# Kernel tuning notes

Measured on AMD Instinct MI355X. Metric: run time of the kernel, lower is better.

## Reference

```python
import jax, jax.numpy as jnp
import numpy as np

B, C, W, H = 4, 256, 64, 64
CQ = C // 8


def setup_inputs() -> dict:
    key = jax.random.key(0)
    ks = jax.random.split(key, 8)
    s = 1.0 / np.sqrt(C)
    return {
        "x": jax.random.normal(ks[0], (B, C, W, H), dtype=jnp.float32),
        "Wq": jax.random.normal(ks[1], (CQ, C), dtype=jnp.float32) * s,
        "bq": jnp.zeros((CQ,), dtype=jnp.float32),
        "Wk": jax.random.normal(ks[2], (CQ, C), dtype=jnp.float32) * s,
        "bk": jnp.zeros((CQ,), dtype=jnp.float32),
        "Wv": jax.random.normal(ks[3], (C, C), dtype=jnp.float32) * s,
        "bv": jnp.zeros((C,), dtype=jnp.float32),
        "gamma": jnp.zeros((1,), dtype=jnp.float32),
    }


def reference(x, Wq, bq, Wk, bk, Wv, bv, gamma):
    b, c, w, h = x.shape
    n = w * h
    xf = x.reshape(b, c, n)  # [B, C, N] flattened spatial
    # 1x1 convs are channel-wise linear maps
    q = jnp.einsum("dc,bcn->bnd", Wq, xf) + bq  # [B, N, C//8]
    k = jnp.einsum("dc,bcn->bdn", Wk, xf) + bk[None, :, None]  # [B, C//8, N]
    v = jnp.einsum("dc,bcn->bdn", Wv, xf) + bv[None, :, None]  # [B, C, N]
    attn = jax.nn.softmax(jnp.einsum("bnd,bdm->bnm", q, k), axis=-1)  # [B, N, N]
    # out[b, c, n] = sum_m v[b, c, m] * attn[b, n, m]
    out = jnp.einsum("bdm,bnm->bdn", v, attn).reshape(b, c, w, h)
    return gamma[0] * out + x
```

## Files before the change

kernel.cpp:

```cpp
#include <hip/hip_runtime.h>
#include <hip/hip_bf16.h>

#define CC 256
#define NN 4096
#define CQ 32
#define LOG2E 1.4426950408889634f

using short4v = __attribute__((ext_vector_type(4))) short;
using short8 = __attribute__((ext_vector_type(8))) short;
using f32x4  = __attribute__((ext_vector_type(4))) float;

static __device__ __forceinline__ short f2bf(float f) {
  __hip_bfloat16 h = __float2bfloat16(f);
  return *reinterpret_cast<short*>(&h);
}

__global__ __launch_bounds__(256) void prep_kernel(
    const float* __restrict__ Wq, const float* __restrict__ Wk,
    const float* __restrict__ Wv, __hip_bfloat16* __restrict__ Wf)
{
  int t = blockIdx.x*256 + threadIdx.x;
  int lane = t & 63, frag = t >> 6;
  int tile = frag >> 3, kc = frag & 7;
  int l15 = lane & 15, quad = lane >> 4;
  int R = tile*16 + l15;
  int k0 = kc*32 + quad*8;
  const float* src;
  if (R < 32)       src = Wq + (size_t)R*CC + k0;
  else if (R < 64)  src = Wk + (size_t)(R-32)*CC + k0;
  else              src = Wv + (size_t)(R-64)*CC + k0;
  float4 a = *(const float4*)(src);
  float4 c = *(const float4*)(src + 4);
  short8 o;
  o[0]=f2bf(a.x); o[1]=f2bf(a.y); o[2]=f2bf(a.z); o[3]=f2bf(a.w);
  o[4]=f2bf(c.x); o[5]=f2bf(c.y); o[6]=f2bf(c.z); o[7]=f2bf(c.w);
  *reinterpret_cast<short8*>(reinterpret_cast<short*>(Wf) + (size_t)t*8) = o;
}

__global__ __launch_bounds__(256) void qkv_kernel(
    const float* __restrict__ x, const __hip_bfloat16* __restrict__ Wf,
    const float* __restrict__ bq, const float* __restrict__ bk,
    const float* __restrict__ bv,
    __hip_bfloat16* __restrict__ qb, __hip_bfloat16* __restrict__ kb,
    __hip_bfloat16* __restrict__ vb)
{
  const int b  = blockIdx.y;
  const int n0 = blockIdx.x * 32;
  const int tid = threadIdx.x;
  const int lane = tid & 63;
  const int w = __builtin_amdgcn_readfirstlane(tid >> 6);
  const int l15 = lane & 15, quad = lane >> 4;

  __shared__ __align__(16) short Xl[16*64*8];
  __shared__ __align__(16) short Vr[4][16][32];

  const float* xb = x + (size_t)b*CC*NN;
#pragma unroll
  for (int i = 0; i < 4; i++) {
    int s = tid + 256*i;
    int g = s >> 6, ln = s & 63;
    int nr = g >> 3, kc = g & 7;
    int l15s = ln & 15, quads = ln >> 4;
    int n = n0 + nr*16 + l15s;
    int c0 = kc*32 + quads*8;
    float v[8];
#pragma unroll
    for (int j = 0; j < 8; j++) v[j] = xb[(size_t)(c0 + j)*NN + n];
    short8 sv;
#pragma unroll
    for (int j = 0; j < 8; j++) sv[j] = f2bf(v[j]);
    *reinterpret_cast<short8*>(&Xl[(size_t)s*8]) = sv;
  }
  __syncthreads();

  const short* wfp = reinterpret_cast<const short*>(Wf);
  short* qb_s = reinterpret_cast<short*>(qb) + (size_t)b*NN*CQ;
  short* kb_s = reinterpret_cast<short*>(kb) + (size_t)b*NN*CQ;
  short* vb_s = reinterpret_cast<short*>(vb) + (size_t)b*CC*NN;

#define QKV_TILE(T) { \
    const int t_ = (T); \
    short8 Af[8]; \
    _Pragma("unroll") \
    for (int kc = 0; kc < 8; kc++) \
      Af[kc] = *(const short8*)(wfp + ((size_t)(t_*8 + kc)*64 + lane)*8); \
    f32x4 ac0 = {0.f,0.f,0.f,0.f}, ac1 = {0.f,0.f,0.f,0.f}; \
    _Pragma("unroll") \
    for (int kc = 0; kc < 8; kc++) { \
      short8 B0 = *(const short8*)(&Xl[((     kc)*64 + lane)*8]); \
      short8 B1 = *(const short8*)(&Xl[((8 +  kc)*64 + lane)*8]); \
      ac0 = __builtin_amdgcn_mfma_f32_16x16x32_bf16(Af[kc], B0, ac0, 0,0,0); \
      ac1 = __builtin_amdgcn_mfma_f32_16x16x32_bf16(Af[kc], B1, ac1, 0,0,0); \
    } \
    if (t_ < 2) { \
      int d0 = t_*16 + quad*4; \
      short4v p0, p1; \
      _Pragma("unroll") \
      for (int r = 0; r < 4; r++) { \
        float bb = bq[d0 + r]; \
        p0[r] = f2bf(LOG2E*(ac0[r] + bb)); \
        p1[r] = f2bf(LOG2E*(ac1[r] + bb)); \
      } \
      *(short4v*)(qb_s + (size_t)(n0      + l15)*CQ + d0) = p0; \
      *(short4v*)(qb_s + (size_t)(n0 + 16 + l15)*CQ + d0) = p1; \
    } else if (t_ < 4) { \
      int d0 = (t_-2)*16 + quad*4; \
      short4v p0, p1; \
      _Pragma("unroll") \
      for (int r = 0; r < 4; r++) { \
        float bb = bk[d0 + r]; \
        p0[r] = f2bf(ac0[r] + bb); \
        p1[r] = f2bf(ac1[r] + bb); \
      } \
      *(short4v*)(kb_s + (size_t)(n0      + l15)*CQ + d0) = p0; \
      *(short4v*)(kb_s + (size_t)(n0 + 16 + l15)*CQ + d0) = p1; \
    } else { \
      int rv0 = (t_-4)*16; \
      _Pragma("unroll") \
      for (int r = 0; r < 4; r++) { \
        float bb = bv[rv0 + quad*4 + r]; \
        Vr[w][quad*4 + r][     l15] = f2bf(ac0[r] + bb); \
        Vr[w][quad*4 + r][16 + l15] = f2bf(ac1[r] + bb); \
      } \
      int row = lane >> 2, cb = (lane & 3)*8; \
      short8 tv = *(const short8*)(&Vr[w][row][cb]); \
      *(short8*)(vb_s + (size_t)(rv0 + row)*NN + n0 + cb) = tv; \
    } }

  QKV_TILE(w);
  QKV_TILE(4 + w);
  QKV_TILE(8 + w);
  QKV_TILE(12 + w);
  QKV_TILE(16 + w);
#undef QKV_TILE
}

__global__ __launch_bounds__(512, 2) void attn_kernel(
    const __hip_bfloat16* __restrict__ qb, const __hip_bfloat16* __restrict__ kb,
    const __hip_bfloat16* __restrict__ vb,
    const float* __restrict__ x, const float* __restrict__ gamma,
    float* __restrict__ out)
{
  const int Bk = blockIdx.x;
  const int b = (Bk & 7) >> 1;
  const int n0 = ((Bk >> 3)*2 + (Bk & 1)) * 64;
  const int tid = threadIdx.x;
  const int lane = tid & 63;
  const int w = __builtin_amdgcn_readfirstlane(tid >> 6);
  const int sg = w & 3;
  const int mh = w >> 2;
  const int l15 = lane & 15, quad = lane >> 4;

  __shared__ __align__(16) short Vs[256][72];
  __shared__ __align__(16) short Ps[64][72];
  __shared__ float Lbuf2[2][64];

  const short* qbase = (const short*)qb + (size_t)b*NN*CQ;
  const short* kbase = (const short*)kb + (size_t)b*NN*CQ;
  const short* vbase = (const short*)vb + (size_t)b*CC*NN;

  short8 aq = *(const short8*)(qbase + (size_t)(n0 + sg*16 + l15)*CQ + quad*8);

  const int vr = tid >> 1, sh = tid & 1;

  short8 vf0, vf1, vf2, vf3, kf0, kf1;
#pragma unroll
  for (int j = 0; j < 4; j++) {
    short8 t = *(const short8*)(vbase + (size_t)vr*NN + sh*32 + j*8);
    if (j == 0) vf0 = t; else if (j == 1) vf1 = t; else if (j == 2) vf2 = t; else vf3 = t;
  }
  kf0 = *(const short8*)(kbase + (size_t)(mh*32 +      l15)*CQ + quad*8);
  kf1 = *(const short8*)(kbase + (size_t)(mh*32 + 16 + l15)*CQ + quad*8);
  *(short8*)(&Vs[vr][sh*32 +  0]) = vf0;
  *(short8*)(&Vs[vr][sh*32 +  8]) = vf1;
  *(short8*)(&Vs[vr][sh*32 + 16]) = vf2;
  *(short8*)(&Vs[vr][sh*32 + 24]) = vf3;

  f32x4 acc[4][4];
#pragma unroll
  for (int cg = 0; cg < 4; cg++)
#pragma unroll
    for (int ng = 0; ng < 4; ng++) acc[cg][ng] = (f32x4){0.f,0.f,0.f,0.f};
  float lsum[4] = {0.f,0.f,0.f,0.f};

  __syncthreads();

  for (int T = 0; T < 64; T++) {
    short8 nv0, nv1, nv2, nv3, nk0, nk1;
    if (T < 63) {
      const short* vp = vbase + (size_t)vr*NN + (T+1)*64 + sh*32;
      nv0 = *(const short8*)(vp);
      nv1 = *(const short8*)(vp + 8);
      nv2 = *(const short8*)(vp + 16);
      nv3 = *(const short8*)(vp + 24);
      nk0 = *(const short8*)(kbase + (size_t)((T+1)*64 + mh*32 +      l15)*CQ + quad*8);
      nk1 = *(const short8*)(kbase + (size_t)((T+1)*64 + mh*32 + 16 + l15)*CQ + quad*8);
    }

    f32x4 z = {0.f,0.f,0.f,0.f};
    f32x4 S0 = __builtin_amdgcn_mfma_f32_16x16x32_bf16(aq, kf0, z, 0,0,0);
    f32x4 S1 = __builtin_amdgcn_mfma_f32_16x16x32_bf16(aq, kf1, z, 0,0,0);
#pragma unroll
    for (int r = 0; r < 4; r++) {
      float e0 = __builtin_amdgcn_exp2f(S0[r]);
      float e1 = __builtin_amdgcn_exp2f(S1[r]);
      lsum[r] += e0 + e1;
      Ps[sg*16 + quad*4 + r][mh*32 +      l15] = f2bf(e0);
      Ps[sg*16 + quad*4 + r][mh*32 + 16 + l15] = f2bf(e1);
    }
    __syncthreads();

    short8 ap0 = *(const short8*)(&Ps[     l15][mh*32 + quad*8]);
    short8 ap1 = *(const short8*)(&Ps[16 + l15][mh*32 + quad*8]);
    short8 ap2 = *(const short8*)(&Ps[32 + l15][mh*32 + quad*8]);
    short8 ap3 = *(const short8*)(&Ps[48 + l15][mh*32 + quad*8]);
#pragma unroll
    for (int cg = 0; cg < 4; cg++) {
      short8 av = *(const short8*)(&Vs[sg*64 + cg*16 + l15][mh*32 + quad*8]);
      acc[cg][0] = __builtin_amdgcn_mfma_f32_16x16x32_bf16(av, ap0, acc[cg][0], 0,0,0);
      acc[cg][1] = __builtin_amdgcn_mfma_f32_16x16x32_bf16(av, ap1, acc[cg][1], 0,0,0);
      acc[cg][2] = __builtin_amdgcn_mfma_f32_16x16x32_bf16(av, ap2, acc[cg][2], 0,0,0);
      acc[cg][3] = __builtin_amdgcn_mfma_f32_16x16x32_bf16(av, ap3, acc[cg][3], 0,0,0);
    }
    __syncthreads();

    if (T < 63) {
      *(short8*)(&Vs[vr][sh*32 +  0]) = nv0;
      *(short8*)(&Vs[vr][sh*32 +  8]) = nv1;
      *(short8*)(&Vs[vr][sh*32 + 16]) = nv2;
      *(short8*)(&Vs[vr][sh*32 + 24]) = nv3;
      kf0 = nk0; kf1 = nk1;
    }
  }

#pragma unroll
  for (int r = 0; r < 4; r++) {
    float s = lsum[r];
    s += __shfl_xor(s, 1); s += __shfl_xor(s, 2);
    s += __shfl_xor(s, 4); s += __shfl_xor(s, 8);
    if (l15 == 0) Lbuf2[mh][sg*16 + quad*4 + r] = s;
  }

  float* poolf = reinterpret_cast<float*>(&Vs[0][0]);
  __syncthreads();
#pragma unroll
  for (int g = 0; g < 2; g++) {
    if (mh == 1 && (sg >> 1) == g) {
#pragma unroll
      for (int cg = 0; cg < 4; cg++)
#pragma unroll
        for (int ng = 0; ng < 4; ng++)
#pragma unroll
          for (int r = 0; r < 4; r++)
            poolf[(sg & 1)*4096 + (cg*16 + quad*4 + r)*64 + ng*16 + l15] = acc[cg][ng][r];
    }
    __syncthreads();
    if (mh == 0 && (sg >> 1) == g) {
#pragma unroll
      for (int cg = 0; cg < 4; cg++)
#pragma unroll
        for (int ng = 0; ng < 4; ng++)
#pragma unroll
          for (int r = 0; r < 4; r++)
            acc[cg][ng][r] += poolf[(sg & 1)*4096 + (cg*16 + quad*4 + r)*64 + ng*16 + l15];
    }
    __syncthreads();
  }

  if (mh == 0) {
    const float gm = gamma[0];
    float Lv[4];
#pragma unroll
    for (int ng = 0; ng < 4; ng++)
      Lv[ng] = 1.0f / (Lbuf2[0][ng*16 + l15] + Lbuf2[1][ng*16 + l15]);
#pragma unroll
    for (int cg = 0; cg < 4; cg++) {
#pragma unroll
      for (int ng = 0; ng < 4; ng++) {
#pragma unroll
        for (int r = 0; r < 4; r++) {
          size_t idx = ((size_t)b*CC + sg*64 + cg*16 + quad*4 + r)*NN + n0 + ng*16 + l15;
          out[idx] = gm * acc[cg][ng][r] * Lv[ng] + x[idx];
        }
      }
    }
  }
}

extern "C" void kernel_launch(void* const* d_in, const int* in_sizes, int n_in,
                              void* d_out, int out_size, void* d_ws, size_t ws_size,
                              hipStream_t stream) {
  const float* x     = (const float*)d_in[0];
  const float* Wq    = (const float*)d_in[1];
  const float* bq    = (const float*)d_in[2];
  const float* Wk    = (const float*)d_in[3];
  const float* bk    = (const float*)d_in[4];
  const float* Wv    = (const float*)d_in[5];
  const float* bv    = (const float*)d_in[6];
  const float* gamma = (const float*)d_in[7];
  float* out = (float*)d_out;

  char* ws = (char*)d_ws;
  if (ws_size < (11u << 20)) return;
  __hip_bfloat16* qb = (__hip_bfloat16*)(ws);
  __hip_bfloat16* kb = (__hip_bfloat16*)(ws + (1u << 20));
  __hip_bfloat16* vb = (__hip_bfloat16*)(ws + (2u << 20));
  __hip_bfloat16* Wf = (__hip_bfloat16*)(ws + (10u << 20));

  prep_kernel<<<dim3(40), 256, 0, stream>>>(Wq, Wk, Wv, Wf);
  qkv_kernel<<<dim3(128, 4), 256, 0, stream>>>(x, Wf, bq, bk, bv, qb, kb, vb);
  attn_kernel<<<dim3(256), 512, 0, stream>>>(qb, kb, vb, x, gamma, out);
}
```

Before: 151.6 us.

## Double waves per block in attention and QKV kernels, splitting work further

The attention kernel goes from 8 to 16 waves per block. Each wave now computes scores for 16 key columns instead of 32, and accumulates PV output for half of the 64 query rows. Row sums are reduced from four partial buffers. The QKV projection kernel likewise moves to 512 threads, each wave handling fewer tiles. The intent is better latency hiding and MFMA utilisation, since only about one block lands per CU. The cost is more LDS traffic and barrier participants per tile, plus aggressive launch bounds that may squeeze registers.

```diff
diff --git a/kernel.cpp b/kernel.cpp
--- a/kernel.cpp
+++ b/kernel.cpp
@@ -37,7 +37,7 @@
   *reinterpret_cast<short8*>(reinterpret_cast<short*>(Wf) + (size_t)t*8) = o;
 }
 
-__global__ __launch_bounds__(256) void qkv_kernel(
+__global__ __launch_bounds__(512, 4) void qkv_kernel(
     const float* __restrict__ x, const __hip_bfloat16* __restrict__ Wf,
     const float* __restrict__ bq, const float* __restrict__ bk,
     const float* __restrict__ bv,
@@ -52,12 +52,12 @@
   const int l15 = lane & 15, quad = lane >> 4;
 
   __shared__ __align__(16) short Xl[16*64*8];
-  __shared__ __align__(16) short Vr[4][16][32];
+  __shared__ __align__(16) short Vr[8][16][32];
 
   const float* xb = x + (size_t)b*CC*NN;
 #pragma unroll
-  for (int i = 0; i < 4; i++) {
-    int s = tid + 256*i;
+  for (int i = 0; i < 2; i++) {
+    int s = tid + 512*i;
     int g = s >> 6, ln = s & 63;
     int nr = g >> 3, kc = g & 7;
     int l15s = ln & 15, quads = ln >> 4;
@@ -128,14 +128,12 @@
     } }
 
   QKV_TILE(w);
-  QKV_TILE(4 + w);
   QKV_TILE(8 + w);
-  QKV_TILE(12 + w);
-  QKV_TILE(16 + w);
+  if (w < 4) { QKV_TILE(16 + w); }
 #undef QKV_TILE
 }
 
-__global__ __launch_bounds__(512, 2) void attn_kernel(
+__global__ __launch_bounds__(1024, 4) void attn_kernel(
     const __hip_bfloat16* __restrict__ qb, const __hip_bfloat16* __restrict__ kb,
     const __hip_bfloat16* __restrict__ vb,
     const float* __restrict__ x, const float* __restrict__ gamma,
@@ -148,12 +146,14 @@
   const int lane = tid & 63;
   const int w = __builtin_amdgcn_readfirstlane(tid >> 6);
   const int sg = w & 3;
-  const int mh = w >> 2;
+  const int mh = (w >> 2) & 1;
+  const int ph = w >> 3;
   const int l15 = lane & 15, quad = lane >> 4;
+  const int mbase = mh*32 + ph*16;
 
   __shared__ __align__(16) short Vs[256][72];
   __shared__ __align__(16) short Ps[64][72];
-  __shared__ float Lbuf2[2][64];
+  __shared__ float Lbuf[4][64];
 
   const short* qbase = (const short*)qb + (size_t)b*NN*CQ;
   const short* kbase = (const short*)kb + (size_t)b*NN*CQ;
@@ -161,75 +161,57 @@
 
   short8 aq = *(const short8*)(qbase + (size_t)(n0 + sg*16 + l15)*CQ + quad*8);
 
-  const int vr = tid >> 1, sh = tid & 1;
-
-  short8 vf0, vf1, vf2, vf3, kf0, kf1;
-#pragma unroll
-  for (int j = 0; j < 4; j++) {
-    short8 t = *(const short8*)(vbase + (size_t)vr*NN + sh*32 + j*8);
-    if (j == 0) vf0 = t; else if (j == 1) vf1 = t; else if (j == 2) vf2 = t; else vf3 = t;
-  }
-  kf0 = *(const short8*)(kbase + (size_t)(mh*32 +      l15)*CQ + quad*8);
-  kf1 = *(const short8*)(kbase + (size_t)(mh*32 + 16 + l15)*CQ + quad*8);
-  *(short8*)(&Vs[vr][sh*32 +  0]) = vf0;
-  *(short8*)(&Vs[vr][sh*32 +  8]) = vf1;
-  *(short8*)(&Vs[vr][sh*32 + 16]) = vf2;
-  *(short8*)(&Vs[vr][sh*32 + 24]) = vf3;
-
-  f32x4 acc[4][4];
+  const int vr = tid >> 2, sh = tid & 3;
+
+  short8 vfa, vfb, kf;
+  vfa = *(const short8*)(vbase + (size_t)vr*NN + sh*16);
+  vfb = *(const short8*)(vbase + (size_t)vr*NN + sh*16 + 8);
+  kf  = *(const short8*)(kbase + (size_t)(mbase + l15)*CQ + quad*8);
+  *(short8*)(&Vs[vr][sh*16    ]) = vfa;
+  *(short8*)(&Vs[vr][sh*16 + 8]) = vfb;
+
+  f32x4 acc[4][2];
 #pragma unroll
   for (int cg = 0; cg < 4; cg++)
 #pragma unroll
-    for (int ng = 0; ng < 4; ng++) acc[cg][ng] = (f32x4){0.f,0.f,0.f,0.f};
+    for (int ng = 0; ng < 2; ng++) acc[cg][ng] = (f32x4){0.f,0.f,0.f,0.f};
   float lsum[4] = {0.f,0.f,0.f,0.f};
 
   __syncthreads();
 
   for (int T = 0; T < 64; T++) {
-    short8 nv0, nv1, nv2, nv3, nk0, nk1;
+    short8 nva, nvb, nk;
     if (T < 63) {
-      const short* vp = vbase + (size_t)vr*NN + (T+1)*64 + sh*32;
-      nv0 = *(const short8*)(vp);
-      nv1 = *(const short8*)(vp + 8);
-      nv2 = *(const short8*)(vp + 16);
-      nv3 = *(const short8*)(vp + 24);
-      nk0 = *(const short8*)(kbase + (size_t)((T+1)*64 + mh*32 +      l15)*CQ + quad*8);
-      nk1 = *(const short8*)(kbase + (size_t)((T+1)*64 + mh*32 + 16 + l15)*CQ + quad*8);
+      const short* vp = vbase + (size_t)vr*NN + (T+1)*64 + sh*16;
+      nva = *(const short8*)(vp);
+      nvb = *(const short8*)(vp + 8);
+      nk  = *(const short8*)(kbase + (size_t)((T+1)*64 + mbase + l15)*CQ + quad*8);
     }
 
     f32x4 z = {0.f,0.f,0.f,0.f};
-    f32x4 S0 = __builtin_amdgcn_mfma_f32_16x16x32_bf16(aq, kf0, z, 0,0,0);
-    f32x4 S1 = __builtin_amdgcn_mfma_f32_16x16x32_bf16(aq, kf1, z, 0,0,0);
+    f32x4 S = __builtin_amdgcn_mfma_f32_16x16x32_bf16(aq, kf, z, 0,0,0);
 #pragma unroll
     for (int r = 0; r < 4; r++) {
-      float e0 = __builtin_amdgcn_exp2f(S0[r]);
-      float e1 = __builtin_amdgcn_exp2f(S1[r]);
-      lsum[r] += e0 + e1;
-      Ps[sg*16 + quad*4 + r][mh*32 +      l15] = f2bf(e0);
-      Ps[sg*16 + quad*4 + r][mh*32 + 16 + l15] = f2bf(e1);
-    }
-    __syncthreads();
-
-    short8 ap0 = *(const short8*)(&Ps[     l15][mh*32 + quad*8]);
-    short8 ap1 = *(const short8*)(&Ps[16 + l15][mh*32 + quad*8]);
-    short8 ap2 = *(const short8*)(&Ps[32 + l15][mh*32 + quad*8]);
-    short8 ap3 = *(const short8*)(&Ps[48 + l15][mh*32 + quad*8]);
+      float e = __builtin_amdgcn_exp2f(S[r]);
+      lsum[r] += e;
+      Ps[sg*16 + quad*4 + r][mbase + l15] = f2bf(e);
+    }
+    __syncthreads();
+
+    short8 ap0 = *(const short8*)(&Ps[(ph*2    )*16 + l15][mh*32 + quad*8]);
+    short8 ap1 = *(const short8*)(&Ps[(ph*2 + 1)*16 + l15][mh*32 + quad*8]);
 #pragma unroll
     for (int cg = 0; cg < 4; cg++) {
       short8 av = *(const short8*)(&Vs[sg*64 + cg*16 + l15][mh*32 + quad*8]);
       acc[cg][0] = __builtin_amdgcn_mfma_f32_16x16x32_bf16(av, ap0, acc[cg][0], 0,0,0);
       acc[cg][1] = __builtin_amdgcn_mfma_f32_16x16x32_bf16(av, ap1, acc[cg][1], 0,0,0);
-      acc[cg][2] = __builtin_amdgcn_mfma_f32_16x16x32_bf16(av, ap2, acc[cg][2], 0,0,0);
-      acc[cg][3] = __builtin_amdgcn_mfma_f32_16x16x32_bf16(av, ap3, acc[cg][3], 0,0,0);
     }
     __syncthreads();
 
     if (T < 63) {
-      *(short8*)(&Vs[vr][sh*32 +  0]) = nv0;
-      *(short8*)(&Vs[vr][sh*32 +  8]) = nv1;
-      *(short8*)(&Vs[vr][sh*32 + 16]) = nv2;
-      *(short8*)(&Vs[vr][sh*32 + 24]) = nv3;
-      kf0 = nk0; kf1 = nk1;
+      *(short8*)(&Vs[vr][sh*16    ]) = nva;
+      *(short8*)(&Vs[vr][sh*16 + 8]) = nvb;
+      kf = nk;
     }
   }
 
@@ -238,7 +220,7 @@
     float s = lsum[r];
     s += __shfl_xor(s, 1); s += __shfl_xor(s, 2);
     s += __shfl_xor(s, 4); s += __shfl_xor(s, 8);
-    if (l15 == 0) Lbuf2[mh][sg*16 + quad*4 + r] = s;
+    if (l15 == 0) Lbuf[mh*2 + ph][sg*16 + quad*4 + r] = s;
   }
 
   float* poolf = reinterpret_cast<float*>(&Vs[0][0]);
@@ -249,37 +231,39 @@
 #pragma unroll
       for (int cg = 0; cg < 4; cg++)
 #pragma unroll
-        for (int ng = 0; ng < 4; ng++)
+        for (int ng = 0; ng < 2; ng++)
 #pragma unroll
           for (int r = 0; r < 4; r++)
-            poolf[(sg & 1)*4096 + (cg*16 + quad*4 + r)*64 + ng*16 + l15] = acc[cg][ng][r];
+            poolf[(sg & 1)*4096 + (cg*16 + quad*4 + r)*64 + (ph*2 + ng)*16 + l15] = acc[cg][ng][r];
     }
     __syncthreads();
     if (mh == 0 && (sg >> 1) == g) {
 #pragma unroll
       for (int cg = 0; cg < 4; cg++)
 #pragma unroll
-        for (int ng = 0; ng < 4; ng++)
+        for (int ng = 0; ng < 2; ng++)
 #pragma unroll
           for (int r = 0; r < 4; r++)
-            acc[cg][ng][r] += poolf[(sg & 1)*4096 + (cg*16 + quad*4 + r)*64 + ng*16 + l15];
+            acc[cg][ng][r] += poolf[(sg & 1)*4096 + (cg*16 + quad*4 + r)*64 + (ph*2 + ng)*16 + l15];
     }
     __syncthreads();
   }
 
   if (mh == 0) {
     const float gm = gamma[0];
-    float Lv[4];
-#pragma unroll
-    for (int ng = 0; ng < 4; ng++)
-      Lv[ng] = 1.0f / (Lbuf2[0][ng*16 + l15] + Lbuf2[1][ng*16 + l15]);
+    float Lv[2];
+#pragma unroll
+    for (int ng = 0; ng < 2; ng++) {
+      int n = (ph*2 + ng)*16 + l15;
+      Lv[ng] = 1.0f / (Lbuf[0][n] + Lbuf[1][n] + Lbuf[2][n] + Lbuf[3][n]);
+    }
 #pragma unroll
     for (int cg = 0; cg < 4; cg++) {
 #pragma unroll
-      for (int ng = 0; ng < 4; ng++) {
+      for (int ng = 0; ng < 2; ng++) {
 #pragma unroll
         for (int r = 0; r < 4; r++) {
-          size_t idx = ((size_t)b*CC + sg*64 + cg*16 + quad*4 + r)*NN + n0 + ng*16 + l15;
+          size_t idx = ((size_t)b*CC + sg*64 + cg*16 + quad*4 + r)*NN + n0 + (ph*2 + ng)*16 + l15;
           out[idx] = gm * acc[cg][ng][r] * Lv[ng] + x[idx];
         }
       }
@@ -308,6 +292,6 @@
   __hip_bfloat16* Wf = (__hip_bfloat16*)(ws + (10u << 20));
 
   prep_kernel<<<dim3(40), 256, 0, stream>>>(Wq, Wk, Wv, Wf);
-  qkv_kernel<<<dim3(128, 4), 256, 0, stream>>>(x, Wf, bq, bk, bv, qb, kb, vb);
-  attn_kernel<<<dim3(256), 512, 0, stream>>>(qb, kb, vb, x, gamma, out);
-}
+  qkv_kernel<<<dim3(128, 4), 512, 0, stream>>>(x, Wf, bq, bk, bv, qb, kb, vb);
+  attn_kernel<<<dim3(256), 1024, 0, stream>>>(qb, kb, vb, x, gamma, out);
+}
```

Measured after the change: 148.0 us. 1.02x faster.

## Transpose score MFMA for packed P stores, widen QKV blocks to 512 threads

Applied to the files above, without the earlier changes.

The attention kernel now swaps the MFMA operands when computing scores, so each lane holds four consecutive key columns for one query row. That lets it write a packed short4 into the padded P tile instead of eight scalar LDS stores, and cuts the row-sum reduction to a single register with two shuffles. The LDS row pitch changes from 72 to 76 shorts to alter the bank mapping. The QKV projection kernel moves to 512 threads with 8 waves, so each wave handles fewer output tiles and the x staging loop is shorter. The new pitch could change bank conflicts on the short8 reads, and the larger QKV block must still fit the register budget.

```diff
diff --git a/kernel.cpp b/kernel.cpp
--- a/kernel.cpp
+++ b/kernel.cpp
@@ -37,7 +37,7 @@
   *reinterpret_cast<short8*>(reinterpret_cast<short*>(Wf) + (size_t)t*8) = o;
 }
 
-__global__ __launch_bounds__(256) void qkv_kernel(
+__global__ __launch_bounds__(512, 4) void qkv_kernel(
     const float* __restrict__ x, const __hip_bfloat16* __restrict__ Wf,
     const float* __restrict__ bq, const float* __restrict__ bk,
     const float* __restrict__ bv,
@@ -52,12 +52,12 @@
   const int l15 = lane & 15, quad = lane >> 4;
 
   __shared__ __align__(16) short Xl[16*64*8];
-  __shared__ __align__(16) short Vr[4][16][32];
+  __shared__ __align__(16) short Vr[8][16][32];
 
   const float* xb = x + (size_t)b*CC*NN;
 #pragma unroll
-  for (int i = 0; i < 4; i++) {
-    int s = tid + 256*i;
+  for (int i = 0; i < 2; i++) {
+    int s = tid + 512*i;
     int g = s >> 6, ln = s & 63;
     int nr = g >> 3, kc = g & 7;
     int l15s = ln & 15, quads = ln >> 4;
@@ -128,10 +128,8 @@
     } }
 
   QKV_TILE(w);
-  QKV_TILE(4 + w);
   QKV_TILE(8 + w);
-  QKV_TILE(12 + w);
-  QKV_TILE(16 + w);
+  if (w < 4) { QKV_TILE(16 + w); }
 #undef QKV_TILE
 }
 
@@ -151,9 +149,9 @@
   const int mh = w >> 2;
   const int l15 = lane & 15, quad = lane >> 4;
 
-  __shared__ __align__(16) short Vs[256][72];
-  __shared__ __align__(16) short Ps[64][72];
-  __shared__ float Lbuf2[2][64];
+  __shared__ __align__(16) short Vs[256][76];
+  __shared__ __align__(16) short Ps[64][76];
+  __shared__ float Lbuf[2][64];
 
   const short* qbase = (const short*)qb + (size_t)b*NN*CQ;
   const short* kbase = (const short*)kb + (size_t)b*NN*CQ;
@@ -162,6 +160,9 @@
   short8 aq = *(const short8*)(qbase + (size_t)(n0 + sg*16 + l15)*CQ + quad*8);
 
   const int vr = tid >> 1, sh = tid & 1;
+
+  short* pdst0 = &Ps[sg*16 + l15][mh*32 +      quad*4];
+  short* pdst1 = &Ps[sg*16 + l15][mh*32 + 16 + quad*4];
 
   short8 vf0, vf1, vf2, vf3, kf0, kf1;
 #pragma unroll
@@ -181,7 +182,7 @@
   for (int cg = 0; cg < 4; cg++)
 #pragma unroll
     for (int ng = 0; ng < 4; ng++) acc[cg][ng] = (f32x4){0.f,0.f,0.f,0.f};
-  float lsum[4] = {0.f,0.f,0.f,0.f};
+  float lsum = 0.f;
 
   __syncthreads();
 
@@ -198,15 +199,20 @@
     }
 
     f32x4 z = {0.f,0.f,0.f,0.f};
-    f32x4 S0 = __builtin_amdgcn_mfma_f32_16x16x32_bf16(aq, kf0, z, 0,0,0);
-    f32x4 S1 = __builtin_amdgcn_mfma_f32_16x16x32_bf16(aq, kf1, z, 0,0,0);
-#pragma unroll
-    for (int r = 0; r < 4; r++) {
-      float e0 = __builtin_amdgcn_exp2f(S0[r]);
-      float e1 = __builtin_amdgcn_exp2f(S1[r]);
-      lsum[r] += e0 + e1;
-      Ps[sg*16 + quad*4 + r][mh*32 +      l15] = f2bf(e0);
-      Ps[sg*16 + quad*4 + r][mh*32 + 16 + l15] = f2bf(e1);
+    f32x4 S0 = __builtin_amdgcn_mfma_f32_16x16x32_bf16(kf0, aq, z, 0,0,0);
+    f32x4 S1 = __builtin_amdgcn_mfma_f32_16x16x32_bf16(kf1, aq, z, 0,0,0);
+    {
+      short4v pk0, pk1;
+#pragma unroll
+      for (int r = 0; r < 4; r++) {
+        float e0 = __builtin_amdgcn_exp2f(S0[r]);
+        float e1 = __builtin_amdgcn_exp2f(S1[r]);
+        lsum += e0 + e1;
+        pk0[r] = f2bf(e0);
+        pk1[r] = f2bf(e1);
+      }
+      *(short4v*)(pdst0) = pk0;
+      *(short4v*)(pdst1) = pk1;
     }
     __syncthreads();
 
@@ -233,12 +239,10 @@
     }
   }
 
-#pragma unroll
-  for (int r = 0; r < 4; r++) {
-    float s = lsum[r];
-    s += __shfl_xor(s, 1); s += __shfl_xor(s, 2);
-    s += __shfl_xor(s, 4); s += __shfl_xor(s, 8);
-    if (l15 == 0) Lbuf2[mh][sg*16 + quad*4 + r] = s;
+  {
+    float s = lsum;
+    s += __shfl_xor(s, 16); s += __shfl_xor(s, 32);
+    if (quad == 0) Lbuf[mh][sg*16 + l15] = s;
   }
 
   float* poolf = reinterpret_cast<float*>(&Vs[0][0]);
@@ -271,8 +275,10 @@
     const float gm = gamma[0];
     float Lv[4];
 #pragma unroll
-    for (int ng = 0; ng < 4; ng++)
-      Lv[ng] = 1.0f / (Lbuf2[0][ng*16 + l15] + Lbuf2[1][ng*16 + l15]);
+    for (int ng = 0; ng < 4; ng++) {
+      int n = ng*16 + l15;
+      Lv[ng] = 1.0f / (Lbuf[0][n] + Lbuf[1][n]);
+    }
 #pragma unroll
     for (int cg = 0; cg < 4; cg++) {
 #pragma unroll
@@ -308,6 +314,6 @@
   __hip_bfloat16* Wf = (__hip_bfloat16*)(ws + (10u << 20));
 
   prep_kernel<<<dim3(40), 256, 0, stream>>>(Wq, Wk, Wv, Wf);
-  qkv_kernel<<<dim3(128, 4), 256, 0, stream>>>(x, Wf, bq, bk, bv, qb, kb, vb);
+  qkv_kernel<<<dim3(128, 4), 512, 0, stream>>>(x, Wf, bq, bk, bv, qb, kb, vb);
   attn_kernel<<<dim3(256), 512, 0, stream>>>(qb, kb, vb, x, gamma, out);
 }
```

Result: no change. 149.5 us (-1.4%).
